# Kernel tuning notes

Measured on AMD Instinct MI355X. Metric: run time of the kernel, lower is better.

Reference implementation:

```python
import jax, jax.numpy as jnp
import numpy as np
from jax import lax

V, D, H, HR = 32000, 512, 1024, 2
T_SRC, T_TGT, T_REF, B, NREF = 128, 128, 32, 64, 4


def _gru_scan(x_emb, lengths, h0, Wih, Whh, bih, bhh):
    """Masked GRU over padded [T,B,D]; equivalent to torch pack->GRU->unpack.
    Returns (outputs [T,B,h] zeroed past lengths, final hidden [B,h])."""
    T = x_emb.shape[0]
    xW = jnp.einsum('tbd,gd->tbg', x_emb, Wih) + bih  # [T,B,3h] input-gate preacts

    def step(h, inp):
        xw, t = inp
        hw = h @ Whh.T + bhh
        xr, xz, xn = jnp.split(xw, 3, axis=-1)
        hr, hz, hn = jnp.split(hw, 3, axis=-1)
        r = jax.nn.sigmoid(xr + hr)
        z = jax.nn.sigmoid(xz + hz)
        n = jnp.tanh(xn + r * hn)
        h_new = (1.0 - z) * n + z * h
        m = (t < lengths)[:, None]
        h_next = jnp.where(m, h_new, h)   # freeze hidden past length (packing)
        out = jnp.where(m, h_new, 0.0)    # unpack pads with zeros
        return h_next, out

    hT, outs = lax.scan(step, h0, (xW, jnp.arange(T)))
    return outs, hT


def setup_inputs() -> dict:
    key = jax.random.key(0)
    ks = jax.random.split(key, 32)

    def u(k, shape, fan):
        lim = 1.0 / np.sqrt(fan)
        return jax.random.uniform(k, shape, jnp.float32, -lim, lim)

    inp = {}
    inp['tgt'] = jax.random.randint(ks[0], (T_TGT, B), 0, V)
    inp['tgt_lengths'] = jax.random.randint(ks[1], (B,), 1, T_TGT + 1)
    inp['src'] = jax.random.randint(ks[2], (T_SRC, B), 0, V)
    inp['src_lengths'] = jax.random.randint(ks[3], (B,), 1, T_SRC + 1)
    inp['ref_ids'] = jax.random.randint(ks[4], (NREF, T_REF, B), 0, V)
    inp['ref_lengths'] = jax.random.randint(ks[5], (NREF, B), 1, T_REF + 1)
    inp['emb'] = jax.random.normal(ks[6], (V, D), jnp.float32) * 0.02
    inp['src_Wih'] = u(ks[7], (3 * H, D), H)
    inp['src_Whh'] = u(ks[8], (3 * H, H), H)
    inp['src_bih'] = u(ks[9], (3 * H,), H)
    inp['src_bhh'] = u(ks[10], (3 * H,), H)
    inp['tgt_Wih'] = u(ks[11], (3 * H, D), H)
    inp['tgt_Whh'] = u(ks[12], (3 * H, H), H)
    inp['tgt_bih'] = u(ks[13], (3 * H,), H)
    inp['tgt_bhh'] = u(ks[14], (3 * H,), H)
    inp['ref_Wih'] = u(ks[15], (3 * HR, D), HR)
    inp['ref_Whh'] = u(ks[16], (3 * HR, HR), HR)
    inp['ref_bih'] = u(ks[17], (3 * HR,), HR)
    inp['ref_bhh'] = u(ks[18], (3 * HR,), HR)
    inp['p1_W'] = u(ks[19], (64, H), H)
    inp['p1_b'] = u(ks[20], (64,), H)
    inp['p2_W'] = u(ks[21], (2, 64), 64)
    inp['p2_b'] = u(ks[22], (2,), 64)
    return inp


def reference(tgt, tgt_lengths, src, src_lengths, ref_ids, ref_lengths, emb,
              src_Wih, src_Whh, src_bih, src_bhh,
              tgt_Wih, tgt_Whh, tgt_bih, tgt_bhh,
              ref_Wih, ref_Whh, ref_bih, ref_bhh,
              p1_W, p1_b, p2_W, p2_b):
    # --- src encoder ---
    src_emb = emb[src]  # [T_SRC,B,D]
    h0 = jnp.zeros((src.shape[1], src_Whh.shape[1]), emb.dtype)
    _, src_hT = _gru_scan(src_emb, src_lengths, h0, src_Wih, src_Whh, src_bih, src_bhh)

    # --- ref encoders: original loops in Python over the ref list with
    # per-ref sort/pack/tiny-GRU; here vectorized with vmap over NREF.
    # (Output is computed, as torch eager does, but does not feed logits.)
    ref_emb = emb[ref_ids]  # [NREF,T_REF,B,D]
    h0r = jnp.zeros((ref_ids.shape[2], ref_Whh.shape[1]), emb.dtype)
    ref_context, ref_hidden = jax.vmap(
        lambda e, l: _gru_scan(e, l, h0r, ref_Wih, ref_Whh, ref_bih, ref_bhh)
    )(ref_emb, ref_lengths)
    del ref_context, ref_hidden

    # --- tgt decoder initialized from src final hidden ---
    tgt_emb = emb[tgt]
    _, tgt_hT = _gru_scan(tgt_emb, tgt_lengths, src_hT, tgt_Wih, tgt_Whh, tgt_bih, tgt_bhh)

    # --- projection head (dropout = identity in eval) ---
    logits = jnp.tanh(tgt_hT @ p1_W.T + p1_b) @ p2_W.T + p2_b  # [B,2]
    return logits
```

## Files before the change

kernel.cpp:

```cpp
#include <hip/hip_runtime.h>
#include <stdint.h>

typedef short short8 __attribute__((ext_vector_type(8)));
typedef float f32x4 __attribute__((ext_vector_type(4)));
typedef float f32x2 __attribute__((ext_vector_type(2)));
typedef unsigned long long u64;

#define TSEQ   128
#define BATCH  64
#define DIM    512
#define HID    1024
#define G3     3072
#define MROWS  (TSEQ * BATCH)
#define NB     32
#define HB     32
#define RING   32
#define SLOT   (BATCH * (HID / 4) * 8)

__device__ __forceinline__ unsigned short f2bf(float f) {
  union { float f; unsigned u; } v; v.f = f;
  unsigned u = v.u;
  return (unsigned short)((u + 0x7FFFu + ((u >> 16) & 1u)) >> 16);
}

__device__ __forceinline__ short8 pack8(f32x4 a, f32x4 b) {
  short8 r;
  r[0] = (short)f2bf(a.x); r[1] = (short)f2bf(a.y);
  r[2] = (short)f2bf(a.z); r[3] = (short)f2bf(a.w);
  r[4] = (short)f2bf(b.x); r[5] = (short)f2bf(b.y);
  r[6] = (short)f2bf(b.z); r[7] = (short)f2bf(b.w);
  return r;
}

__device__ __forceinline__ u64 packbf4(float a, float b, float c, float d) {
  return (u64)f2bf(a) | ((u64)f2bf(b) << 16) | ((u64)f2bf(c) << 32) | ((u64)f2bf(d) << 48);
}

__device__ __forceinline__ float sigm(float x) { return 1.0f / (1.0f + __expf(-x)); }
__device__ __forceinline__ float tanh_fast(float x) { return 2.0f / (1.0f + __expf(-2.0f * x)) - 1.0f; }

__global__ __launch_bounds__(256) void prep_kernel(
    const int* __restrict__ ids, const float* __restrict__ emb,
    const float* __restrict__ wih, unsigned short* __restrict__ X,
    unsigned short* __restrict__ Wb, unsigned int* bars)
{
  int row = blockIdx.x;
  int tid = threadIdx.x;
  const float* srcp;
  unsigned short* dst;
  if (row < MROWS) {
    srcp = emb + (long)ids[row] * DIM;
    dst  = X + (long)row * DIM;
  } else {
    int wr = row - MROWS;
    srcp = wih + (long)wr * DIM;
    dst  = Wb + (long)wr * DIM;
  }
  int d = tid * 2;
  f32x2 v = *(const f32x2*)(srcp + d);
  unsigned pk = (unsigned)f2bf(v.x) | ((unsigned)f2bf(v.y) << 16);
  *(unsigned*)(dst + d) = pk;
  if (bars != nullptr && row == 0) ((f32x4*)bars)[tid] = (f32x4){};
}

#define BM 128
#define BN 128
#define BK 32

__global__ __launch_bounds__(256) void xw_gemm(
    const unsigned short* __restrict__ X,
    const unsigned short* __restrict__ W,
    const float* __restrict__ bih,
    float* __restrict__ out)
{
  __shared__ unsigned short As[BM * BK];
  __shared__ unsigned short Bs[BN * BK];
  int tid = threadIdx.x;
  int w = tid >> 6, l = tid & 63;
  int m0 = blockIdx.y * BM;
  int n0 = blockIdx.x * BN;
  int wr = w >> 1, wc = w & 1;

  int sr = tid >> 2, skq = tid & 3;
  int sr2 = sr + 64;
  int sgk  = (skq - (sr  >> 1)) & 3;
  int sgk2 = (skq - (sr2 >> 1)) & 3;
  const unsigned short* gA0 = X + (long)(m0 + sr ) * DIM + sgk  * 8;
  const unsigned short* gA1 = X + (long)(m0 + sr2) * DIM + sgk2 * 8;
  const unsigned short* gB0 = W + (long)(n0 + sr ) * DIM + sgk  * 8;
  const unsigned short* gB1 = W + (long)(n0 + sr2) * DIM + sgk2 * 8;
  unsigned short* lA0 = As + sr  * BK + skq * 8;
  unsigned short* lA1 = As + sr2 * BK + skq * 8;
  unsigned short* lB0 = Bs + sr  * BK + skq * 8;
  unsigned short* lB1 = Bs + sr2 * BK + skq * 8;

  f32x4 acc[4][4];
  #pragma unroll
  for (int mt = 0; mt < 4; ++mt)
    #pragma unroll
    for (int nt = 0; nt < 4; ++nt) acc[mt][nt] = (f32x4){};

  short8 va0 = *(const short8*)(gA0);
  short8 va1 = *(const short8*)(gA1);
  short8 vb0 = *(const short8*)(gB0);
  short8 vb1 = *(const short8*)(gB1);

  int fr = l & 15, fk = l >> 4;
  for (int kt = 0; kt < DIM / BK; ++kt) {
    __syncthreads();
    *(short8*)lA0 = va0; *(short8*)lA1 = va1;
    *(short8*)lB0 = vb0; *(short8*)lB1 = vb1;
    __syncthreads();
    if (kt + 1 < DIM / BK) {
      int ko = (kt + 1) * BK;
      va0 = *(const short8*)(gA0 + ko);
      va1 = *(const short8*)(gA1 + ko);
      vb0 = *(const short8*)(gB0 + ko);
      vb1 = *(const short8*)(gB1 + ko);
    }
    short8 af[4], bf[4];
    #pragma unroll
    for (int mt = 0; mt < 4; ++mt) {
      int r = wr * 64 + mt * 16 + fr;
      int slot = ((r >> 1) + fk) & 3;
      af[mt] = *(const short8*)(As + r * BK + slot * 8);
    }
    #pragma unroll
    for (int nt = 0; nt < 4; ++nt) {
      int r = wc * 64 + nt * 16 + fr;
      int slot = ((r >> 1) + fk) & 3;
      bf[nt] = *(const short8*)(Bs + r * BK + slot * 8);
    }
    #pragma unroll
    for (int mt = 0; mt < 4; ++mt)
      #pragma unroll
      for (int nt = 0; nt < 4; ++nt)
        acc[mt][nt] = __builtin_amdgcn_mfma_f32_16x16x32_bf16(af[mt], bf[nt], acc[mt][nt], 0, 0, 0);
  }

  #pragma unroll
  for (int nt = 0; nt < 4; ++nt) {
    int n = n0 + wc * 64 + nt * 16 + fr;
    float bias = bih[n];
    #pragma unroll
    for (int mt = 0; mt < 4; ++mt) {
      int mbase = m0 + wr * 64 + mt * 16 + fk * 4;
      #pragma unroll
      for (int r = 0; r < 4; ++r)
        out[(long)(mbase + r) * G3 + n] = acc[mt][nt][r] + bias;
    }
  }
}

#define MF(a, b, c) __builtin_amdgcn_mfma_f32_16x16x32_bf16(a, b, c, 0, 0, 0)

#define ISSUE(ss, kk) do { \
  asm volatile("global_load_dwordx4 %0, %1, off offset:%2 sc0" \
               : "=v"(bv[ss][0]) : "v"(ad0), "i"((kk) * 64) : "memory"); \
  asm volatile("global_load_dwordx4 %0, %1, off offset:%2 sc0" \
               : "=v"(bv[ss][1]) : "v"(ad1), "i"((kk) * 64) : "memory"); \
  asm volatile("global_load_dwordx4 %0, %1, off offset:%2 sc0" \
               : "=v"(bv[ss][2]) : "v"(ad2), "i"((kk) * 64) : "memory"); \
  asm volatile("global_load_dwordx4 %0, %1, off offset:%2 sc0" \
               : "=v"(bv[ss][3]) : "v"(ad3), "i"((kk) * 64) : "memory"); \
} while (0)

#define MF6(kk, ss, nt) \
  acc[0][nt] = MF(areg[0][kk], bv[ss][nt], acc[0][nt]); \
  acc[1][nt] = MF(areg[1][kk], bv[ss][nt], acc[1][nt]); \
  acc[2][nt] = MF(areg[2][kk], bv[ss][nt], acc[2][nt]); \
  acc[3][nt] = MF(areg[3][kk], bv[ss][nt], acc[3][nt]); \
  acc[4][nt] = MF(areg[4][kk], bv[ss][nt], acc[4][nt]); \
  acc[5][nt] = MF(areg[5][kk], bv[ss][nt], acc[5][nt]);

#define CONS(kk, ss, wn) do { \
  asm volatile("s_waitcnt vmcnt(" #wn ")" ::: "memory"); \
  __builtin_amdgcn_sched_barrier(0); \
  MF6(kk, ss, 0) MF6(kk, ss, 1) MF6(kk, ss, 2) MF6(kk, ss, 3) \
} while (0)

#define CONSI(kk, ss, wn, nk) do { CONS(kk, ss, wn); ISSUE(ss, nk); } while (0)

#define BARRIER_ARRIVE(tgtv) do { \
  asm volatile("s_waitcnt vmcnt(0)" ::: "memory"); \
  __syncthreads(); \
  if (tid == 0) { \
    unsigned fv_ = (unsigned)(tgtv); \
    uint64_t fa_ = (uint64_t)(bar + (((tgtv) & 1) << 5) + blockIdx.x); \
    asm volatile("global_store_dword %0, %1, off sc0 sc1" :: "v"(fa_), "v"(fv_) : "memory"); \
  } \
} while (0)

#define BARRIER_WAIT(tgtv) do { \
  if (tid < NB) { \
    unsigned v_; \
    uint64_t pa_ = (uint64_t)(bar + (((tgtv) & 1) << 5) + tid); \
    do { \
      asm volatile("global_load_dword %0, %1, off sc0 sc1" : "=v"(v_) : "v"(pa_) : "memory"); \
      asm volatile("s_waitcnt vmcnt(0)" ::: "memory"); \
    } while (__any(v_ < (unsigned)(tgtv))); \
  } \
  __syncthreads(); \
} while (0)

__global__ __launch_bounds__(256, 1) void gru_kernel(
    const float* __restrict__ Whh, const float* __restrict__ bhh,
    const float* __restrict__ xw, const int* __restrict__ lengths,
    u64* __restrict__ hbf,
    float* __restrict__ hf32,
    unsigned int* __restrict__ bar, int T, int initzero)
{
  const int tid = threadIdx.x;
  const int w = tid >> 6, l = tid & 63;
  const int fr = l & 15, fk = l >> 4;
  const int U0 = blockIdx.x * HB;

  short8 areg[6][8];
  #pragma unroll
  for (int mt = 0; mt < 6; ++mt) {
    const int m = mt * 16 + fr;
    const int gate = m >> 5, u = m & 31;
    const float* wp = Whh + (size_t)(gate * HID + U0 + u) * HID + w * 256 + fk * 8;
    #pragma unroll
    for (int ksl = 0; ksl < 8; ++ksl) {
      f32x4 a0 = *(const f32x4*)(wp + ksl * 32);
      f32x4 a1 = *(const f32x4*)(wp + ksl * 32 + 4);
      areg[mt][ksl] = pack8(a0, a1);
    }
  }

  const int gb = l;
  const int j0 = w * 8;
  const size_t hoff = (size_t)gb * (HID / 4) + (size_t)(U0 + j0) / 4;
  const int len_b = lengths[gb];

  float h[8];
  #pragma unroll
  for (int j = 0; j < 8; ++j)
    h[j] = initzero ? 0.0f : hf32[(size_t)gb * HID + U0 + j0 + j];

  __shared__ float red2[4][64][100];
  __shared__ float bb[3][32];
  if (tid < 96) bb[tid >> 5][tid & 31] = bhh[(tid >> 5) * HID + U0 + (tid & 31)];

  f32x4 xrv[2], xzv[2], xnv[2];
  #define LOAD_XW(tt) do { \
    const float* xp_ = xw + ((size_t)(tt) * BATCH + gb) * G3 + U0 + j0; \
    xrv[0] = *(const f32x4*)(xp_);            xrv[1] = *(const f32x4*)(xp_ + 4); \
    xzv[0] = *(const f32x4*)(xp_ + HID);      xzv[1] = *(const f32x4*)(xp_ + HID + 4); \
    xnv[0] = *(const f32x4*)(xp_ + 2 * HID);  xnv[1] = *(const f32x4*)(xp_ + 2 * HID + 4); \
  } while (0)

  {
    union { u64 q[2]; f32x4 v4; } pk;
    pk.q[0] = packbf4(h[0], h[1], h[2], h[3]);
    pk.q[1] = packbf4(h[4], h[5], h[6], h[7]);
    uint64_t hw = (uint64_t)(hbf + hoff);
    asm volatile("global_store_dwordx4 %0, %1, off sc0 sc1" :: "v"(hw), "v"(pk.v4) : "memory");
    BARRIER_ARRIVE(1);
    asm volatile("buffer_inv sc1" ::: "memory");
    LOAD_XW(0);
    BARRIER_WAIT(1);
  }

  for (int t = 0; t < T; ++t) {
    asm volatile("s_waitcnt vmcnt(0)" ::: "memory");

    const char* hbase = (const char*)hbf + (size_t)(t & (RING - 1)) * SLOT;
    uint64_t ad0 = (uint64_t)(hbase + (size_t)(fr) * 2048 + w * 512 + fk * 16);
    uint64_t ad1 = ad0 + 16 * 2048;
    uint64_t ad2 = ad0 + 32 * 2048;
    uint64_t ad3 = ad0 + 48 * 2048;

    f32x4 acc[6][4];
    #pragma unroll
    for (int mt = 0; mt < 6; ++mt)
      #pragma unroll
      for (int nt = 0; nt < 4; ++nt) acc[mt][nt] = (f32x4){};

    short8 bv[6][4];
    ISSUE(0, 0); ISSUE(1, 1); ISSUE(2, 2); ISSUE(3, 3); ISSUE(4, 4); ISSUE(5, 5);
    CONSI(0, 0, 20, 6);
    CONSI(1, 1, 20, 7);
    CONS(2, 2, 20);
    CONS(3, 3, 16);
    CONS(4, 4, 12);
    CONS(5, 5, 8);
    CONS(6, 0, 4);
    CONS(7, 1, 0);

    #pragma unroll
    for (int mt = 0; mt < 6; ++mt)
      #pragma unroll
      for (int nt = 0; nt < 4; ++nt)
        *(f32x4*)&red2[w][nt * 16 + fr][mt * 16 + fk * 4] = acc[mt][nt];
    __syncthreads();

    #define RD4(s, row) (*(const f32x4*)&red2[s][gb][row])
    f32x4 sr_[2], sz_[2], sn_[2];
    #pragma unroll
    for (int hh = 0; hh < 2; ++hh) {
      const int rbase = j0 + hh * 4;
      sr_[hh] = RD4(0, rbase)      + RD4(1, rbase)      + RD4(2, rbase)      + RD4(3, rbase)      + *(const f32x4*)&bb[0][rbase];
      sz_[hh] = RD4(0, 32 + rbase) + RD4(1, 32 + rbase) + RD4(2, 32 + rbase) + RD4(3, 32 + rbase) + *(const f32x4*)&bb[1][rbase];
      sn_[hh] = RD4(0, 64 + rbase) + RD4(1, 64 + rbase) + RD4(2, 64 + rbase) + RD4(3, 64 + rbase) + *(const f32x4*)&bb[2][rbase];
    }

    const int upd = (t < len_b);
    #pragma unroll
    for (int j = 0; j < 8; ++j) {
      float rr = sigm(xrv[j >> 2][j & 3] + sr_[j >> 2][j & 3]);
      float zz = sigm(xzv[j >> 2][j & 3] + sz_[j >> 2][j & 3]);
      float nn = tanh_fast(xnv[j >> 2][j & 3] + rr * sn_[j >> 2][j & 3]);
      float cc = (1.0f - zz) * nn + zz * h[j];
      h[j] = upd ? cc : h[j];
    }

    if (t + 1 < T) {
      union { u64 q[2]; f32x4 v4; } pk;
      pk.q[0] = packbf4(h[0], h[1], h[2], h[3]);
      pk.q[1] = packbf4(h[4], h[5], h[6], h[7]);
      uint64_t hw = (uint64_t)((char*)hbf + (size_t)((t + 1) & (RING - 1)) * SLOT + hoff * 8);
      asm volatile("global_store_dwordx4 %0, %1, off sc0 sc1" :: "v"(hw), "v"(pk.v4) : "memory");
      BARRIER_ARRIVE(t + 2);
      LOAD_XW(t + 1);
      BARRIER_WAIT(t + 2);
      if (((t + 1) & (RING - 1)) == 0)
        asm volatile("buffer_inv sc1" ::: "memory");
    }
  }

  #pragma unroll
  for (int j = 0; j < 8; ++j)
    hf32[(size_t)gb * HID + U0 + j0 + j] = h[j];
}

__global__ __launch_bounds__(256) void head_kernel(
    const float* __restrict__ hf32, const float* __restrict__ p1W,
    const float* __restrict__ p1b, const float* __restrict__ p2W,
    const float* __restrict__ p2b, float* __restrict__ outp)
{
  int b = blockIdx.x;
  int tid = threadIdx.x;
  __shared__ float hrow[HID];
  __shared__ float red[4][64];
  __shared__ float s1[64];
  for (int d = tid; d < HID; d += 256) hrow[d] = hf32[(long)b * HID + d];
  __syncthreads();
  int j = tid & 63, q = tid >> 6;
  const float* wrow = p1W + (long)j * HID + q * 256;
  float s = 0.0f;
  for (int k = 0; k < 256; ++k) s += hrow[q * 256 + k] * wrow[k];
  red[q][j] = s;
  __syncthreads();
  if (tid < 64) {
    float v = red[0][tid] + red[1][tid] + red[2][tid] + red[3][tid] + p1b[tid];
    s1[tid] = tanh_fast(v);
  }
  __syncthreads();
  if (tid < 2) {
    float a = p2b[tid];
    for (int k = 0; k < 64; ++k) a += s1[k] * p2W[tid * 64 + k];
    outp[b * 2 + tid] = a;
  }
}

extern "C" void kernel_launch(void* const* d_in, const int* in_sizes, int n_in,
                              void* d_out, int out_size, void* d_ws, size_t ws_size,
                              hipStream_t stream) {
  const int*   tgt_ids = (const int*)d_in[0];
  const int*   tgt_len = (const int*)d_in[1];
  const int*   src_ids = (const int*)d_in[2];
  const int*   src_len = (const int*)d_in[3];
  const float* emb  = (const float*)d_in[6];
  const float* sWih = (const float*)d_in[7];
  const float* sWhh = (const float*)d_in[8];
  const float* sbih = (const float*)d_in[9];
  const float* sbhh = (const float*)d_in[10];
  const float* tWih = (const float*)d_in[11];
  const float* tWhh = (const float*)d_in[12];
  const float* tbih = (const float*)d_in[13];
  const float* tbhh = (const float*)d_in[14];
  const float* p1W  = (const float*)d_in[19];
  const float* p1b  = (const float*)d_in[20];
  const float* p2W  = (const float*)d_in[21];
  const float* p2b  = (const float*)d_in[22];

  char* ws = (char*)d_ws;
  size_t off = 0;
  float* xw = (float*)(ws + off);                   off += (size_t)MROWS * G3 * 4;
  unsigned short* X  = (unsigned short*)(ws + off); off += (size_t)MROWS * DIM * 2;
  unsigned short* Wb = (unsigned short*)(ws + off); off += (size_t)G3 * DIM * 2;
  float* hf32 = (float*)(ws + off);                 off += (size_t)BATCH * HID * 4;
  unsigned int* bars = (unsigned int*)(ws + off);   off += 8192;
  if (ws_size < off) return;
  u64* hbf = (u64*)X;

  const int PREP_BLOCKS = MROWS + G3;

  prep_kernel<<<PREP_BLOCKS, 256, 0, stream>>>(src_ids, emb, sWih, X, Wb, bars);
  xw_gemm<<<dim3(G3 / BN, MROWS / BM), 256, 0, stream>>>(X, Wb, sbih, xw);
  gru_kernel<<<NB, 256, 0, stream>>>(sWhh, sbhh, xw, src_len, hbf, hf32, bars, TSEQ, 1);
  prep_kernel<<<PREP_BLOCKS, 256, 0, stream>>>(tgt_ids, emb, tWih, X, Wb, nullptr);
  xw_gemm<<<dim3(G3 / BN, MROWS / BM), 256, 0, stream>>>(X, Wb, tbih, xw);
  gru_kernel<<<NB, 256, 0, stream>>>(tWhh, tbhh, xw, tgt_len, hbf, hf32, bars + 1024, TSEQ, 0);
  head_kernel<<<BATCH, 256, 0, stream>>>(hf32, p1W, p1b, p2W, p2b, (float*)d_out);
}
```

Baseline: 2.163 ms.

## Split GRU recurrent gate rows across twice as many waves per block

```diff
diff --git a/kernel.cpp b/kernel.cpp
--- a/kernel.cpp
+++ b/kernel.cpp
@@ -60,7 +60,10 @@
   f32x2 v = *(const f32x2*)(srcp + d);
   unsigned pk = (unsigned)f2bf(v.x) | ((unsigned)f2bf(v.y) << 16);
   *(unsigned*)(dst + d) = pk;
-  if (bars != nullptr && row == 0) ((f32x4*)bars)[tid] = (f32x4){};
+  if (bars != nullptr && row == 0) {
+    ((f32x4*)bars)[tid] = (f32x4){};
+    ((f32x4*)bars)[256 + tid] = (f32x4){};
+  }
 }
 
 #define BM 128
@@ -165,18 +168,15 @@
                : "=v"(bv[ss][3]) : "v"(ad3), "i"((kk) * 64) : "memory"); \
 } while (0)
 
-#define MF6(kk, ss, nt) \
+#define MF3(kk, ss, nt) \
   acc[0][nt] = MF(areg[0][kk], bv[ss][nt], acc[0][nt]); \
   acc[1][nt] = MF(areg[1][kk], bv[ss][nt], acc[1][nt]); \
-  acc[2][nt] = MF(areg[2][kk], bv[ss][nt], acc[2][nt]); \
-  acc[3][nt] = MF(areg[3][kk], bv[ss][nt], acc[3][nt]); \
-  acc[4][nt] = MF(areg[4][kk], bv[ss][nt], acc[4][nt]); \
-  acc[5][nt] = MF(areg[5][kk], bv[ss][nt], acc[5][nt]);
+  acc[2][nt] = MF(areg[2][kk], bv[ss][nt], acc[2][nt]);
 
 #define CONS(kk, ss, wn) do { \
   asm volatile("s_waitcnt vmcnt(" #wn ")" ::: "memory"); \
   __builtin_amdgcn_sched_barrier(0); \
-  MF6(kk, ss, 0) MF6(kk, ss, 1) MF6(kk, ss, 2) MF6(kk, ss, 3) \
+  MF3(kk, ss, 0) MF3(kk, ss, 1) MF3(kk, ss, 2) MF3(kk, ss, 3) \
 } while (0)
 
 #define CONSI(kk, ss, wn, nk) do { CONS(kk, ss, wn); ISSUE(ss, nk); } while (0)
@@ -203,7 +203,7 @@
   __syncthreads(); \
 } while (0)
 
-__global__ __launch_bounds__(256, 1) void gru_kernel(
+__global__ __launch_bounds__(512, 2) void gru_kernel(
     const float* __restrict__ Whh, const float* __restrict__ bhh,
     const float* __restrict__ xw, const int* __restrict__ lengths,
     u64* __restrict__ hbf,
@@ -213,14 +213,15 @@
   const int tid = threadIdx.x;
   const int w = tid >> 6, l = tid & 63;
   const int fr = l & 15, fk = l >> 4;
+  const int ko = w & 3, mo = w >> 2;
   const int U0 = blockIdx.x * HB;
 
-  short8 areg[6][8];
+  short8 areg[3][8];
   #pragma unroll
-  for (int mt = 0; mt < 6; ++mt) {
-    const int m = mt * 16 + fr;
+  for (int mt = 0; mt < 3; ++mt) {
+    const int m = mo * 48 + mt * 16 + fr;
     const int gate = m >> 5, u = m & 31;
-    const float* wp = Whh + (size_t)(gate * HID + U0 + u) * HID + w * 256 + fk * 8;
+    const float* wp = Whh + (size_t)(gate * HID + U0 + u) * HID + ko * 256 + fk * 8;
     #pragma unroll
     for (int ksl = 0; ksl < 8; ++ksl) {
       f32x4 a0 = *(const f32x4*)(wp + ksl * 32);
@@ -229,34 +230,32 @@
     }
   }
 
-  const int gb = l;
-  const int j0 = w * 8;
+  const int gb = tid & 63;
+  const int j0 = (tid >> 6) * 4;
   const size_t hoff = (size_t)gb * (HID / 4) + (size_t)(U0 + j0) / 4;
   const int len_b = lengths[gb];
 
-  float h[8];
+  float h[4];
   #pragma unroll
-  for (int j = 0; j < 8; ++j)
+  for (int j = 0; j < 4; ++j)
     h[j] = initzero ? 0.0f : hf32[(size_t)gb * HID + U0 + j0 + j];
 
   __shared__ float red2[4][64][100];
   __shared__ float bb[3][32];
   if (tid < 96) bb[tid >> 5][tid & 31] = bhh[(tid >> 5) * HID + U0 + (tid & 31)];
 
-  f32x4 xrv[2], xzv[2], xnv[2];
+  f32x4 xrv, xzv, xnv;
   #define LOAD_XW(tt) do { \
     const float* xp_ = xw + ((size_t)(tt) * BATCH + gb) * G3 + U0 + j0; \
-    xrv[0] = *(const f32x4*)(xp_);            xrv[1] = *(const f32x4*)(xp_ + 4); \
-    xzv[0] = *(const f32x4*)(xp_ + HID);      xzv[1] = *(const f32x4*)(xp_ + HID + 4); \
-    xnv[0] = *(const f32x4*)(xp_ + 2 * HID);  xnv[1] = *(const f32x4*)(xp_ + 2 * HID + 4); \
+    xrv = *(const f32x4*)(xp_); \
+    xzv = *(const f32x4*)(xp_ + HID); \
+    xnv = *(const f32x4*)(xp_ + 2 * HID); \
   } while (0)
 
   {
-    union { u64 q[2]; f32x4 v4; } pk;
-    pk.q[0] = packbf4(h[0], h[1], h[2], h[3]);
-    pk.q[1] = packbf4(h[4], h[5], h[6], h[7]);
+    u64 pk = packbf4(h[0], h[1], h[2], h[3]);
     uint64_t hw = (uint64_t)(hbf + hoff);
-    asm volatile("global_store_dwordx4 %0, %1, off sc0 sc1" :: "v"(hw), "v"(pk.v4) : "memory");
+    asm volatile("global_store_dwordx2 %0, %1, off sc0 sc1" :: "v"(hw), "v"(pk) : "memory");
     BARRIER_ARRIVE(1);
     asm volatile("buffer_inv sc1" ::: "memory");
     LOAD_XW(0);
@@ -267,61 +266,54 @@
     asm volatile("s_waitcnt vmcnt(0)" ::: "memory");
 
     const char* hbase = (const char*)hbf + (size_t)(t & (RING - 1)) * SLOT;
-    uint64_t ad0 = (uint64_t)(hbase + (size_t)(fr) * 2048 + w * 512 + fk * 16);
+    uint64_t ad0 = (uint64_t)(hbase + (size_t)(fr) * 2048 + ko * 512 + fk * 16);
     uint64_t ad1 = ad0 + 16 * 2048;
     uint64_t ad2 = ad0 + 32 * 2048;
     uint64_t ad3 = ad0 + 48 * 2048;
 
-    f32x4 acc[6][4];
-    #pragma unroll
-    for (int mt = 0; mt < 6; ++mt)
+    f32x4 acc[3][4];
+    #pragma unroll
+    for (int mt = 0; mt < 3; ++mt)
       #pragma unroll
       for (int nt = 0; nt < 4; ++nt) acc[mt][nt] = (f32x4){};
 
-    short8 bv[6][4];
-    ISSUE(0, 0); ISSUE(1, 1); ISSUE(2, 2); ISSUE(3, 3); ISSUE(4, 4); ISSUE(5, 5);
-    CONSI(0, 0, 20, 6);
-    CONSI(1, 1, 20, 7);
-    CONS(2, 2, 20);
-    CONS(3, 3, 16);
-    CONS(4, 4, 12);
-    CONS(5, 5, 8);
+    short8 bv[3][4];
+    ISSUE(0, 0); ISSUE(1, 1); ISSUE(2, 2);
+    CONSI(0, 0, 8, 3);
+    CONSI(1, 1, 8, 4);
+    CONSI(2, 2, 8, 5);
+    CONSI(3, 0, 8, 6);
+    CONSI(4, 1, 8, 7);
+    CONS(5, 2, 8);
     CONS(6, 0, 4);
     CONS(7, 1, 0);
 
     #pragma unroll
-    for (int mt = 0; mt < 6; ++mt)
+    for (int mt = 0; mt < 3; ++mt)
       #pragma unroll
       for (int nt = 0; nt < 4; ++nt)
-        *(f32x4*)&red2[w][nt * 16 + fr][mt * 16 + fk * 4] = acc[mt][nt];
+        *(f32x4*)&red2[ko][nt * 16 + fr][mo * 48 + mt * 16 + fk * 4] = acc[mt][nt];
     __syncthreads();
 
     #define RD4(s, row) (*(const f32x4*)&red2[s][gb][row])
-    f32x4 sr_[2], sz_[2], sn_[2];
-    #pragma unroll
-    for (int hh = 0; hh < 2; ++hh) {
-      const int rbase = j0 + hh * 4;
-      sr_[hh] = RD4(0, rbase)      + RD4(1, rbase)      + RD4(2, rbase)      + RD4(3, rbase)      + *(const f32x4*)&bb[0][rbase];
-      sz_[hh] = RD4(0, 32 + rbase) + RD4(1, 32 + rbase) + RD4(2, 32 + rbase) + RD4(3, 32 + rbase) + *(const f32x4*)&bb[1][rbase];
-      sn_[hh] = RD4(0, 64 + rbase) + RD4(1, 64 + rbase) + RD4(2, 64 + rbase) + RD4(3, 64 + rbase) + *(const f32x4*)&bb[2][rbase];
-    }
+    f32x4 sr_ = RD4(0, j0)      + RD4(1, j0)      + RD4(2, j0)      + RD4(3, j0)      + *(const f32x4*)&bb[0][j0];
+    f32x4 sz_ = RD4(0, 32 + j0) + RD4(1, 32 + j0) + RD4(2, 32 + j0) + RD4(3, 32 + j0) + *(const f32x4*)&bb[1][j0];
+    f32x4 sn_ = RD4(0, 64 + j0) + RD4(1, 64 + j0) + RD4(2, 64 + j0) + RD4(3, 64 + j0) + *(const f32x4*)&bb[2][j0];
 
     const int upd = (t < len_b);
     #pragma unroll
-    for (int j = 0; j < 8; ++j) {
-      float rr = sigm(xrv[j >> 2][j & 3] + sr_[j >> 2][j & 3]);
-      float zz = sigm(xzv[j >> 2][j & 3] + sz_[j >> 2][j & 3]);
-      float nn = tanh_fast(xnv[j >> 2][j & 3] + rr * sn_[j >> 2][j & 3]);
+    for (int j = 0; j < 4; ++j) {
+      float rr = sigm(xrv[j] + sr_[j]);
+      float zz = sigm(xzv[j] + sz_[j]);
+      float nn = tanh_fast(xnv[j] + rr * sn_[j]);
       float cc = (1.0f - zz) * nn + zz * h[j];
       h[j] = upd ? cc : h[j];
     }
 
     if (t + 1 < T) {
-      union { u64 q[2]; f32x4 v4; } pk;
-      pk.q[0] = packbf4(h[0], h[1], h[2], h[3]);
-      pk.q[1] = packbf4(h[4], h[5], h[6], h[7]);
+      u64 pk = packbf4(h[0], h[1], h[2], h[3]);
       uint64_t hw = (uint64_t)((char*)hbf + (size_t)((t + 1) & (RING - 1)) * SLOT + hoff * 8);
-      asm volatile("global_store_dwordx4 %0, %1, off sc0 sc1" :: "v"(hw), "v"(pk.v4) : "memory");
+      asm volatile("global_store_dwordx2 %0, %1, off sc0 sc1" :: "v"(hw), "v"(pk) : "memory");
       BARRIER_ARRIVE(t + 2);
       LOAD_XW(t + 1);
       BARRIER_WAIT(t + 2);
@@ -331,7 +323,7 @@
   }
 
   #pragma unroll
-  for (int j = 0; j < 8; ++j)
+  for (int j = 0; j < 4; ++j)
     hf32[(size_t)gb * HID + U0 + j0 + j] = h[j];
 }
 
@@ -400,9 +392,9 @@
 
   prep_kernel<<<PREP_BLOCKS, 256, 0, stream>>>(src_ids, emb, sWih, X, Wb, bars);
   xw_gemm<<<dim3(G3 / BN, MROWS / BM), 256, 0, stream>>>(X, Wb, sbih, xw);
-  gru_kernel<<<NB, 256, 0, stream>>>(sWhh, sbhh, xw, src_len, hbf, hf32, bars, TSEQ, 1);
+  gru_kernel<<<NB, 512, 0, stream>>>(sWhh, sbhh, xw, src_len, hbf, hf32, bars, TSEQ, 1);
   prep_kernel<<<PREP_BLOCKS, 256, 0, stream>>>(tgt_ids, emb, tWih, X, Wb, nullptr);
   xw_gemm<<<dim3(G3 / BN, MROWS / BM), 256, 0, stream>>>(X, Wb, tbih, xw);
-  gru_kernel<<<NB, 256, 0, stream>>>(tWhh, tbhh, xw, tgt_len, hbf, hf32, bars + 1024, TSEQ, 0);
+  gru_kernel<<<NB, 512, 0, stream>>>(tWhh, tbhh, xw, tgt_len, hbf, hf32, bars + 1024, TSEQ, 0);
   head_kernel<<<BATCH, 256, 0, stream>>>(hf32, p1W, p1b, p2W, p2b, (float*)d_out);
 }
```

After: 2.897 ms. 1.34x slower.
